# Kernel tuning notes

Hardware: AMD Instinct MI355X
Metric: run time of the kernel (lower is better)

Reference implementation:

```python
import jax, jax.numpy as jnp
import numpy as np

N_NODES = 100000
N_EDGES = 600000
D_IN = 128
D_HID = 128
BLOCKS = 3


def setup_inputs() -> dict:
    key = jax.random.key(0)
    ks = jax.random.split(key, 8)
    x = jax.random.normal(ks[0], (N_NODES, D_IN), dtype=jnp.float32)
    edge_index = jax.random.randint(ks[1], (2, N_EDGES), 0, N_NODES, dtype=jnp.int64)
    s = 1.0 / np.sqrt(D_HID)
    # MLP params per GIN block: Linear1 [hid,in], Linear2 [hid,hid] (torch layout: [out,in])
    W1 = jax.random.uniform(ks[2], (BLOCKS, D_HID, D_IN), jnp.float32, -s, s)
    b1 = jax.random.uniform(ks[3], (BLOCKS, D_HID), jnp.float32, -s, s)
    W2 = jax.random.uniform(ks[4], (BLOCKS, D_HID, D_HID), jnp.float32, -s, s)
    b2 = jax.random.uniform(ks[5], (BLOCKS, D_HID), jnp.float32, -s, s)
    Wf = jax.random.uniform(ks[6], (1, D_HID), jnp.float32, -s, s)
    bf = jax.random.uniform(ks[7], (1,), jnp.float32, -s, s)
    return {"x": x, "edge_index": edge_index, "W1": W1, "b1": b1,
            "W2": W2, "b2": b2, "Wf": Wf, "bf": bf}


def reference(x, edge_index, W1, b1, W2, b2, Wf, bf):
    src, dst = edge_index[0], edge_index[1]
    n = x.shape[0]
    h = x
    for i in range(BLOCKS):
        # GIN aggregation: (1+eps)*x_i + sum over neighbors, eps=0
        agg = jax.ops.segment_sum(h[src], dst, num_segments=n)  # [N, d]
        z = h + agg
        # 2-layer MLP inside GINConv
        z = jax.nn.relu(z @ W1[i].T + b1[i])
        z = z @ W2[i].T + b2[i]
        # outer ReLU applied in Net.forward
        h = jax.nn.relu(z)
    return h @ Wf.T + bf  # [N, 1]
```

## Files before the change

kernel.cpp:

```cpp
#include <hip/hip_runtime.h>
#include <hip/hip_bf16.h>

typedef __bf16 bf16x8 __attribute__((ext_vector_type(8)));
typedef __bf16 bf16x2 __attribute__((ext_vector_type(2)));
typedef float f32x4 __attribute__((ext_vector_type(4)));

#define NN 100000
#define DD 128
#define NE 600000
#define SLOTS 64

__global__ void convert_bf16(const float4* __restrict__ in, __bf16* __restrict__ out, int n4) {
    int i = blockIdx.x * blockDim.x + threadIdx.x;
    if (i >= n4) return;
    float4 v = in[i];
    bf16x2 a, b;
    a[0] = (__bf16)v.x; a[1] = (__bf16)v.y;
    b[0] = (__bf16)v.z; b[1] = (__bf16)v.w;
    *reinterpret_cast<bf16x2*>(out + (size_t)i * 4)     = a;
    *reinterpret_cast<bf16x2*>(out + (size_t)i * 4 + 2) = b;
}

__global__ void clear_ints(int* __restrict__ p, int n) {
    int i = blockIdx.x * blockDim.x + threadIdx.x;
    if (i < n) p[i] = 0;
}

__global__ void fill_slots(const int* __restrict__ src, const int* __restrict__ dst,
                           int* __restrict__ deg, int* __restrict__ slots, int nE) {
    int e = blockIdx.x * blockDim.x + threadIdx.x;
    if (e >= nE) return;
    int d = dst[e];
    int pos = atomicAdd(&deg[d], 1);
    if (pos < SLOTS) slots[(size_t)d * SLOTS + pos] = src[e];
}

__global__ __launch_bounds__(256) void aggregate(const __bf16* __restrict__ h,
                                                 const int* __restrict__ deg,
                                                 const int* __restrict__ slots,
                                                 __bf16* __restrict__ z, int N) {
    const int tid = threadIdx.x;
    const int grp = tid >> 4;
    const int lm  = tid & 15;
    const int n = blockIdx.x * 16 + grp;
    if (n >= N) return;
    const int off = lm * 8;

    const bf16x8 sv = *reinterpret_cast<const bf16x8*>(h + (size_t)n * DD + off);
    float acc[8];
#pragma unroll
    for (int i = 0; i < 8; ++i) acc[i] = (float)sv[i];

    int d = deg[n]; if (d > 32) d = 32;
    const int* sl = slots + (size_t)n * SLOTS;
    const int d1 = d < 16 ? d : 16;
    int myidx = (lm < d1) ? sl[lm] : 0;

    int j = 0;
    if (j + 8 <= d1) {
        int s[8];
#pragma unroll
        for (int q = 0; q < 8; ++q) s[q] = __shfl(myidx, j + q, 16);
        bf16x8 v[8];
#pragma unroll
        for (int q = 0; q < 8; ++q) v[q] = *reinterpret_cast<const bf16x8*>(h + (size_t)s[q] * DD + off);
#pragma unroll
        for (int q = 0; q < 8; ++q)
#pragma unroll
            for (int i = 0; i < 8; ++i) acc[i] += (float)v[q][i];
        j += 8;
    }
    if (j + 4 <= d1) {
        int s[4];
#pragma unroll
        for (int q = 0; q < 4; ++q) s[q] = __shfl(myidx, j + q, 16);
        bf16x8 v[4];
#pragma unroll
        for (int q = 0; q < 4; ++q) v[q] = *reinterpret_cast<const bf16x8*>(h + (size_t)s[q] * DD + off);
#pragma unroll
        for (int q = 0; q < 4; ++q)
#pragma unroll
            for (int i = 0; i < 8; ++i) acc[i] += (float)v[q][i];
        j += 4;
    }
    for (; j < d1; ++j) {
        int s = __shfl(myidx, j, 16);
        bf16x8 v = *reinterpret_cast<const bf16x8*>(h + (size_t)s * DD + off);
#pragma unroll
        for (int i = 0; i < 8; ++i) acc[i] += (float)v[i];
    }

    if (d > 16) {
        const int d2 = d - 16;
        int myidx2 = (lm < d2) ? sl[16 + lm] : 0;
        j = 0;
        if (j + 8 <= d2) {
            int s[8];
#pragma unroll
            for (int q = 0; q < 8; ++q) s[q] = __shfl(myidx2, j + q, 16);
            bf16x8 v[8];
#pragma unroll
            for (int q = 0; q < 8; ++q) v[q] = *reinterpret_cast<const bf16x8*>(h + (size_t)s[q] * DD + off);
#pragma unroll
            for (int q = 0; q < 8; ++q)
#pragma unroll
                for (int i = 0; i < 8; ++i) acc[i] += (float)v[q][i];
            j += 8;
        }
        if (j + 4 <= d2) {
            int s[4];
#pragma unroll
            for (int q = 0; q < 4; ++q) s[q] = __shfl(myidx2, j + q, 16);
            bf16x8 v[4];
#pragma unroll
            for (int q = 0; q < 4; ++q) v[q] = *reinterpret_cast<const bf16x8*>(h + (size_t)s[q] * DD + off);
#pragma unroll
            for (int q = 0; q < 4; ++q)
#pragma unroll
                for (int i = 0; i < 8; ++i) acc[i] += (float)v[q][i];
            j += 4;
        }
        for (; j < d2; ++j) {
            int s = __shfl(myidx2, j, 16);
            bf16x8 v = *reinterpret_cast<const bf16x8*>(h + (size_t)s * DD + off);
#pragma unroll
            for (int i = 0; i < 8; ++i) acc[i] += (float)v[i];
        }
    }

    bf16x8 o;
#pragma unroll
    for (int i = 0; i < 8; ++i) o[i] = (__bf16)acc[i];
    *reinterpret_cast<bf16x8*>(z + (size_t)n * DD + off) = o;
}

template<bool LAST>
__global__ __launch_bounds__(512) void mlp_fused(const __bf16* __restrict__ A,
                                                 const float* __restrict__ W1,
                                                 const float* __restrict__ b1,
                                                 const float* __restrict__ W2,
                                                 const float* __restrict__ b2,
                                                 const float* __restrict__ Wf,
                                                 const float* __restrict__ bfp,
                                                 __bf16* __restrict__ Hout,
                                                 float* __restrict__ out, int N) {
    __shared__ __bf16 w1l[128 * 136];
    __shared__ __bf16 w2l[128 * 136];
    __shared__ __bf16 tl[128 * 136];
    const int tid = threadIdx.x;

    for (int i = tid; i < 128 * 128; i += 512) {
        int r = i >> 7, c = i & 127;
        w1l[r * 136 + c] = (__bf16)W1[i];
        w2l[r * 136 + c] = (__bf16)W2[i];
    }
    __syncthreads();

    const int wave = tid >> 6;
    const int lane = tid & 63;
    const int lm = lane & 15;
    const int kg = lane >> 4;
    const int rowL = wave * 16;
    const int row0 = blockIdx.x * 128 + rowL;

    f32x4 acc[8];
#pragma unroll
    for (int c = 0; c < 8; ++c) acc[c] = (f32x4){0.f, 0.f, 0.f, 0.f};

#pragma unroll
    for (int kk = 0; kk < 4; ++kk) {
        const int kbase = kk * 32 + kg * 8;
        int r = row0 + lm;
        if (r >= N) r = N - 1;
        const bf16x8 a = *reinterpret_cast<const bf16x8*>(A + (size_t)r * DD + kbase);
#pragma unroll
        for (int c = 0; c < 8; ++c) {
            const bf16x8 b = *reinterpret_cast<const bf16x8*>(&w1l[(c * 16 + lm) * 136 + kbase]);
            acc[c] = __builtin_amdgcn_mfma_f32_16x16x32_bf16(a, b, acc[c], 0, 0, 0);
        }
    }
#pragma unroll
    for (int c = 0; c < 8; ++c) {
        const int col = c * 16 + lm;
        const float bv = b1[col];
#pragma unroll
        for (int j = 0; j < 4; ++j) {
            float v = acc[c][j] + bv;
            tl[(rowL + kg * 4 + j) * 136 + col] = (__bf16)(v > 0.f ? v : 0.f);
        }
    }
    __syncthreads();

    f32x4 acc2[8];
#pragma unroll
    for (int c = 0; c < 8; ++c) acc2[c] = (f32x4){0.f, 0.f, 0.f, 0.f};

#pragma unroll
    for (int kk = 0; kk < 4; ++kk) {
        const int kbase = kk * 32 + kg * 8;
        const bf16x8 a2 = *reinterpret_cast<const bf16x8*>(&tl[(rowL + lm) * 136 + kbase]);
#pragma unroll
        for (int c = 0; c < 8; ++c) {
            const bf16x8 b = *reinterpret_cast<const bf16x8*>(&w2l[(c * 16 + lm) * 136 + kbase]);
            acc2[c] = __builtin_amdgcn_mfma_f32_16x16x32_bf16(a2, b, acc2[c], 0, 0, 0);
        }
    }

    if (!LAST) {
        __syncthreads();
#pragma unroll
        for (int c = 0; c < 8; ++c) {
            const int col = c * 16 + lm;
            const float bv = b2[col];
#pragma unroll
            for (int j = 0; j < 4; ++j) {
                float v = acc2[c][j] + bv;
                tl[(rowL + kg * 4 + j) * 136 + col] = (__bf16)(v > 0.f ? v : 0.f);
            }
        }
        __syncthreads();
        for (int i = tid; i < 128 * 16; i += 512) {
            int r = i >> 4, cc = (i & 15) * 8;
            int gr = blockIdx.x * 128 + r;
            if (gr < N) {
                bf16x8 v = *reinterpret_cast<const bf16x8*>(&tl[r * 136 + cc]);
                *reinterpret_cast<bf16x8*>(Hout + (size_t)gr * DD + cc) = v;
            }
        }
    } else {
        float wv[8];
#pragma unroll
        for (int c = 0; c < 8; ++c) wv[c] = Wf[c * 16 + lm];
        const float bias0 = bfp[0];
#pragma unroll
        for (int j = 0; j < 4; ++j) {
            float p = 0.f;
#pragma unroll
            for (int c = 0; c < 8; ++c) {
                const int col = c * 16 + lm;
                float v = acc2[c][j] + b2[col];
                p += (v > 0.f ? v : 0.f) * wv[c];
            }
            p += __shfl_xor(p, 1, 64);
            p += __shfl_xor(p, 2, 64);
            p += __shfl_xor(p, 4, 64);
            p += __shfl_xor(p, 8, 64);
            int row = row0 + kg * 4 + j;
            if (lm == 0 && row < N) out[row] = p + bias0;
        }
    }
}

extern "C" void kernel_launch(void* const* d_in, const int* in_sizes, int n_in,
                              void* d_out, int out_size, void* d_ws, size_t ws_size,
                              hipStream_t stream) {
    const float* x  = (const float*)d_in[0];
    const int*   ei = (const int*)d_in[1];
    const float* W1 = (const float*)d_in[2];
    const float* b1 = (const float*)d_in[3];
    const float* W2 = (const float*)d_in[4];
    const float* b2 = (const float*)d_in[5];
    const float* Wf = (const float*)d_in[6];
    const float* bf = (const float*)d_in[7];
    float* out = (float*)d_out;

    const int* src = ei;
    const int* dst = ei + NE;

    __bf16* Zb   = (__bf16*)d_ws;
    __bf16* Hb   = Zb + (size_t)NN * DD;
    __bf16* Xb   = Hb + (size_t)NN * DD;
    int*  slots  = (int*)(Xb + (size_t)NN * DD);
    int*  deg    = slots + (size_t)NN * SLOTS;

    const int aggGrid = (NN + 15) / 16;
    const int mlpGrid = (NN + 127) / 128;
    const int n4 = NN * DD / 4;

    convert_bf16<<<(n4 + 255) / 256, 256, 0, stream>>>((const float4*)x, Xb, n4);
    clear_ints<<<(NN + 255) / 256, 256, 0, stream>>>(deg, NN);
    fill_slots<<<(NE + 255) / 256, 256, 0, stream>>>(src, dst, deg, slots, NE);

    aggregate<<<aggGrid, 256, 0, stream>>>(Xb, deg, slots, Zb, NN);
    mlp_fused<false><<<mlpGrid, 512, 0, stream>>>(Zb, W1, b1, W2, b2, Wf, bf, Hb, out, NN);
    aggregate<<<aggGrid, 256, 0, stream>>>(Hb, deg, slots, Zb, NN);
    mlp_fused<false><<<mlpGrid, 512, 0, stream>>>(Zb, W1 + 128 * 128, b1 + 128, W2 + 128 * 128, b2 + 128,
                                                  Wf, bf, Hb, out, NN);
    aggregate<<<aggGrid, 256, 0, stream>>>(Hb, deg, slots, Zb, NN);
    mlp_fused<true><<<mlpGrid, 512, 0, stream>>>(Zb, W1 + 2 * 128 * 128, b1 + 2 * 128, W2 + 2 * 128 * 128,
                                                 b2 + 2 * 128, Wf, bf, Hb, out, NN);
}
```

Measured before the change: 228.5 us.

## Fuse neighbor aggregation into GIN MLP kernel and prelaunch bf16 weight conversion

Merges the separate aggregate and MLP kernels into one gin_block kernel. Each block gathers neighbor sums for its 128 rows straight into shared memory, which removes the Z round trip through global memory and half the launches. Weights are converted to bf16 once by a separate kernel and read from global/L2 in the MFMA loops instead of being staged in LDS. This shrinks LDS use so more blocks can be resident, at the cost of uncoalesced global weight loads. The degree counters are also padded to a stride of 16 ints to spread the atomics, and the slot count is halved from 64 to 32.

Result: slower. 318.4 us (+39.3%).

```diff
diff --git a/kernel.cpp b/kernel.cpp
--- a/kernel.cpp
+++ b/kernel.cpp
@@ -8,7 +8,8 @@
 #define NN 100000
 #define DD 128
 #define NE 600000
-#define SLOTS 64
+#define SLOTS 32
+#define DEGSTRIDE 16
 
 __global__ void convert_bf16(const float4* __restrict__ in, __bf16* __restrict__ out, int n4) {
     int i = blockIdx.x * blockDim.x + threadIdx.x;
@@ -21,138 +22,137 @@
     *reinterpret_cast<bf16x2*>(out + (size_t)i * 4 + 2) = b;
 }
 
+__global__ void convert_w(const float* __restrict__ W1, const float* __restrict__ W2,
+                          __bf16* __restrict__ W1b, __bf16* __restrict__ W2b, int n) {
+    int i = blockIdx.x * blockDim.x + threadIdx.x;
+    if (i < n) { W1b[i] = (__bf16)W1[i]; W2b[i] = (__bf16)W2[i]; }
+}
+
 __global__ void clear_ints(int* __restrict__ p, int n) {
     int i = blockIdx.x * blockDim.x + threadIdx.x;
     if (i < n) p[i] = 0;
 }
 
 __global__ void fill_slots(const int* __restrict__ src, const int* __restrict__ dst,
-                           int* __restrict__ deg, int* __restrict__ slots, int nE) {
+                           int* __restrict__ degp, int* __restrict__ slots, int nE) {
     int e = blockIdx.x * blockDim.x + threadIdx.x;
     if (e >= nE) return;
     int d = dst[e];
-    int pos = atomicAdd(&deg[d], 1);
+    int pos = atomicAdd(&degp[(size_t)d * DEGSTRIDE], 1);
     if (pos < SLOTS) slots[(size_t)d * SLOTS + pos] = src[e];
 }
 
-__global__ __launch_bounds__(256) void aggregate(const __bf16* __restrict__ h,
-                                                 const int* __restrict__ deg,
-                                                 const int* __restrict__ slots,
-                                                 __bf16* __restrict__ z, int N) {
-    const int tid = threadIdx.x;
-    const int grp = tid >> 4;
-    const int lm  = tid & 15;
-    const int n = blockIdx.x * 16 + grp;
-    if (n >= N) return;
-    const int off = lm * 8;
-
-    const bf16x8 sv = *reinterpret_cast<const bf16x8*>(h + (size_t)n * DD + off);
-    float acc[8];
-#pragma unroll
-    for (int i = 0; i < 8; ++i) acc[i] = (float)sv[i];
-
-    int d = deg[n]; if (d > 32) d = 32;
-    const int* sl = slots + (size_t)n * SLOTS;
-    const int d1 = d < 16 ? d : 16;
-    int myidx = (lm < d1) ? sl[lm] : 0;
-
-    int j = 0;
-    if (j + 8 <= d1) {
-        int s[8];
-#pragma unroll
-        for (int q = 0; q < 8; ++q) s[q] = __shfl(myidx, j + q, 16);
-        bf16x8 v[8];
-#pragma unroll
-        for (int q = 0; q < 8; ++q) v[q] = *reinterpret_cast<const bf16x8*>(h + (size_t)s[q] * DD + off);
-#pragma unroll
-        for (int q = 0; q < 8; ++q)
-#pragma unroll
-            for (int i = 0; i < 8; ++i) acc[i] += (float)v[q][i];
-        j += 8;
-    }
-    if (j + 4 <= d1) {
-        int s[4];
-#pragma unroll
-        for (int q = 0; q < 4; ++q) s[q] = __shfl(myidx, j + q, 16);
-        bf16x8 v[4];
-#pragma unroll
-        for (int q = 0; q < 4; ++q) v[q] = *reinterpret_cast<const bf16x8*>(h + (size_t)s[q] * DD + off);
-#pragma unroll
-        for (int q = 0; q < 4; ++q)
-#pragma unroll
-            for (int i = 0; i < 8; ++i) acc[i] += (float)v[q][i];
-        j += 4;
-    }
-    for (; j < d1; ++j) {
-        int s = __shfl(myidx, j, 16);
-        bf16x8 v = *reinterpret_cast<const bf16x8*>(h + (size_t)s * DD + off);
-#pragma unroll
-        for (int i = 0; i < 8; ++i) acc[i] += (float)v[i];
-    }
-
-    if (d > 16) {
-        const int d2 = d - 16;
-        int myidx2 = (lm < d2) ? sl[16 + lm] : 0;
-        j = 0;
-        if (j + 8 <= d2) {
-            int s[8];
-#pragma unroll
-            for (int q = 0; q < 8; ++q) s[q] = __shfl(myidx2, j + q, 16);
-            bf16x8 v[8];
-#pragma unroll
-            for (int q = 0; q < 8; ++q) v[q] = *reinterpret_cast<const bf16x8*>(h + (size_t)s[q] * DD + off);
-#pragma unroll
-            for (int q = 0; q < 8; ++q)
-#pragma unroll
-                for (int i = 0; i < 8; ++i) acc[i] += (float)v[q][i];
-            j += 8;
-        }
-        if (j + 4 <= d2) {
-            int s[4];
-#pragma unroll
-            for (int q = 0; q < 4; ++q) s[q] = __shfl(myidx2, j + q, 16);
-            bf16x8 v[4];
-#pragma unroll
-            for (int q = 0; q < 4; ++q) v[q] = *reinterpret_cast<const bf16x8*>(h + (size_t)s[q] * DD + off);
-#pragma unroll
-            for (int q = 0; q < 4; ++q)
-#pragma unroll
-                for (int i = 0; i < 8; ++i) acc[i] += (float)v[q][i];
-            j += 4;
-        }
-        for (; j < d2; ++j) {
-            int s = __shfl(myidx2, j, 16);
-            bf16x8 v = *reinterpret_cast<const bf16x8*>(h + (size_t)s * DD + off);
-#pragma unroll
-            for (int i = 0; i < 8; ++i) acc[i] += (float)v[i];
-        }
-    }
-
-    bf16x8 o;
-#pragma unroll
-    for (int i = 0; i < 8; ++i) o[i] = (__bf16)acc[i];
-    *reinterpret_cast<bf16x8*>(z + (size_t)n * DD + off) = o;
-}
-
 template<bool LAST>
-__global__ __launch_bounds__(512) void mlp_fused(const __bf16* __restrict__ A,
-                                                 const float* __restrict__ W1,
-                                                 const float* __restrict__ b1,
-                                                 const float* __restrict__ W2,
-                                                 const float* __restrict__ b2,
-                                                 const float* __restrict__ Wf,
-                                                 const float* __restrict__ bfp,
-                                                 __bf16* __restrict__ Hout,
-                                                 float* __restrict__ out, int N) {
-    __shared__ __bf16 w1l[128 * 136];
-    __shared__ __bf16 w2l[128 * 136];
+__global__ __launch_bounds__(512, 4) void gin_block(const __bf16* __restrict__ Hin,
+                                                    const int* __restrict__ degp,
+                                                    const int* __restrict__ slots,
+                                                    const __bf16* __restrict__ W1b,
+                                                    const float* __restrict__ b1,
+                                                    const __bf16* __restrict__ W2b,
+                                                    const float* __restrict__ b2,
+                                                    const float* __restrict__ Wf,
+                                                    const float* __restrict__ bfp,
+                                                    __bf16* __restrict__ Hout,
+                                                    float* __restrict__ out, int N) {
     __shared__ __bf16 tl[128 * 136];
     const int tid = threadIdx.x;
 
-    for (int i = tid; i < 128 * 128; i += 512) {
-        int r = i >> 7, c = i & 127;
-        w1l[r * 136 + c] = (__bf16)W1[i];
-        w2l[r * 136 + c] = (__bf16)W2[i];
+    {
+        const int grp = tid >> 4;
+        const int lg  = tid & 15;
+        const int off = lg * 8;
+#pragma unroll
+        for (int it = 0; it < 4; ++it) {
+            const int ln = grp + (it << 5);
+            const int n = blockIdx.x * 128 + ln;
+            float acc[8] = {0.f,0.f,0.f,0.f,0.f,0.f,0.f,0.f};
+            if (n < N) {
+                const bf16x8 sv = *reinterpret_cast<const bf16x8*>(Hin + (size_t)n * DD + off);
+#pragma unroll
+                for (int i = 0; i < 8; ++i) acc[i] = (float)sv[i];
+
+                int d = degp[(size_t)n * DEGSTRIDE]; if (d > SLOTS) d = SLOTS;
+                const int* sl = slots + (size_t)n * SLOTS;
+                const int d1 = d < 16 ? d : 16;
+                int myidx = (lg < d1) ? sl[lg] : 0;
+
+                int j = 0;
+                if (j + 8 <= d1) {
+                    int s[8];
+#pragma unroll
+                    for (int q = 0; q < 8; ++q) s[q] = __shfl(myidx, j + q, 16);
+                    bf16x8 v[8];
+#pragma unroll
+                    for (int q = 0; q < 8; ++q) v[q] = *reinterpret_cast<const bf16x8*>(Hin + (size_t)s[q] * DD + off);
+#pragma unroll
+                    for (int q = 0; q < 8; ++q)
+#pragma unroll
+                        for (int i = 0; i < 8; ++i) acc[i] += (float)v[q][i];
+                    j += 8;
+                }
+                if (j + 4 <= d1) {
+                    int s[4];
+#pragma unroll
+                    for (int q = 0; q < 4; ++q) s[q] = __shfl(myidx, j + q, 16);
+                    bf16x8 v[4];
+#pragma unroll
+                    for (int q = 0; q < 4; ++q) v[q] = *reinterpret_cast<const bf16x8*>(Hin + (size_t)s[q] * DD + off);
+#pragma unroll
+                    for (int q = 0; q < 4; ++q)
+#pragma unroll
+                        for (int i = 0; i < 8; ++i) acc[i] += (float)v[q][i];
+                    j += 4;
+                }
+                for (; j < d1; ++j) {
+                    int s = __shfl(myidx, j, 16);
+                    bf16x8 v = *reinterpret_cast<const bf16x8*>(Hin + (size_t)s * DD + off);
+#pragma unroll
+                    for (int i = 0; i < 8; ++i) acc[i] += (float)v[i];
+                }
+
+                if (d > 16) {
+                    const int d2 = d - 16;
+                    int myidx2 = (lg < d2) ? sl[16 + lg] : 0;
+                    j = 0;
+                    if (j + 8 <= d2) {
+                        int s[8];
+#pragma unroll
+                        for (int q = 0; q < 8; ++q) s[q] = __shfl(myidx2, j + q, 16);
+                        bf16x8 v[8];
+#pragma unroll
+                        for (int q = 0; q < 8; ++q) v[q] = *reinterpret_cast<const bf16x8*>(Hin + (size_t)s[q] * DD + off);
+#pragma unroll
+                        for (int q = 0; q < 8; ++q)
+#pragma unroll
+                            for (int i = 0; i < 8; ++i) acc[i] += (float)v[q][i];
+                        j += 8;
+                    }
+                    if (j + 4 <= d2) {
+                        int s[4];
+#pragma unroll
+                        for (int q = 0; q < 4; ++q) s[q] = __shfl(myidx2, j + q, 16);
+                        bf16x8 v[4];
+#pragma unroll
+                        for (int q = 0; q < 4; ++q) v[q] = *reinterpret_cast<const bf16x8*>(Hin + (size_t)s[q] * DD + off);
+#pragma unroll
+                        for (int q = 0; q < 4; ++q)
+#pragma unroll
+                            for (int i = 0; i < 8; ++i) acc[i] += (float)v[q][i];
+                        j += 4;
+                    }
+                    for (; j < d2; ++j) {
+                        int s = __shfl(myidx2, j, 16);
+                        bf16x8 v = *reinterpret_cast<const bf16x8*>(Hin + (size_t)s * DD + off);
+#pragma unroll
+                        for (int i = 0; i < 8; ++i) acc[i] += (float)v[i];
+                    }
+                }
+            }
+            bf16x8 o;
+#pragma unroll
+            for (int i = 0; i < 8; ++i) o[i] = (__bf16)acc[i];
+            *reinterpret_cast<bf16x8*>(&tl[ln * 136 + off]) = o;
+        }
     }
     __syncthreads();
 
@@ -170,15 +170,14 @@
 #pragma unroll
     for (int kk = 0; kk < 4; ++kk) {
         const int kbase = kk * 32 + kg * 8;
-        int r = row0 + lm;
-        if (r >= N) r = N - 1;
-        const bf16x8 a = *reinterpret_cast<const bf16x8*>(A + (size_t)r * DD + kbase);
+        const bf16x8 a = *reinterpret_cast<const bf16x8*>(&tl[(rowL + lm) * 136 + kbase]);
 #pragma unroll
         for (int c = 0; c < 8; ++c) {
-            const bf16x8 b = *reinterpret_cast<const bf16x8*>(&w1l[(c * 16 + lm) * 136 + kbase]);
+            const bf16x8 b = *reinterpret_cast<const bf16x8*>(W1b + (size_t)(c * 16 + lm) * DD + kbase);
             acc[c] = __builtin_amdgcn_mfma_f32_16x16x32_bf16(a, b, acc[c], 0, 0, 0);
         }
     }
+    __syncthreads();
 #pragma unroll
     for (int c = 0; c < 8; ++c) {
         const int col = c * 16 + lm;
@@ -201,7 +200,7 @@
         const bf16x8 a2 = *reinterpret_cast<const bf16x8*>(&tl[(rowL + lm) * 136 + kbase]);
 #pragma unroll
         for (int c = 0; c < 8; ++c) {
-            const bf16x8 b = *reinterpret_cast<const bf16x8*>(&w2l[(c * 16 + lm) * 136 + kbase]);
+            const bf16x8 b = *reinterpret_cast<const bf16x8*>(W2b + (size_t)(c * 16 + lm) * DD + kbase);
             acc2[c] = __builtin_amdgcn_mfma_f32_16x16x32_bf16(a2, b, acc2[c], 0, 0, 0);
         }
     }
@@ -267,26 +266,29 @@
     const int* src = ei;
     const int* dst = ei + NE;
 
-    __bf16* Zb   = (__bf16*)d_ws;
-    __bf16* Hb   = Zb + (size_t)NN * DD;
-    __bf16* Xb   = Hb + (size_t)NN * DD;
-    int*  slots  = (int*)(Xb + (size_t)NN * DD);
-    int*  deg    = slots + (size_t)NN * SLOTS;
-
-    const int aggGrid = (NN + 15) / 16;
-    const int mlpGrid = (NN + 127) / 128;
+    __bf16* Xb  = (__bf16*)d_ws;
+    __bf16* Ha  = Xb + (size_t)NN * DD;
+    __bf16* Hc  = Ha + (size_t)NN * DD;
+    __bf16* W1b = Hc + (size_t)NN * DD;
+    __bf16* W2b = W1b + 3 * DD * DD;
+    int* slots  = (int*)(W2b + 3 * DD * DD);
+    int* degp   = slots + (size_t)NN * SLOTS;
+
+    const int ginGrid = (NN + 127) / 128;
     const int n4 = NN * DD / 4;
+    const int nw = 3 * DD * DD;
 
     convert_bf16<<<(n4 + 255) / 256, 256, 0, stream>>>((const float4*)x, Xb, n4);
-    clear_ints<<<(NN + 255) / 256, 256, 0, stream>>>(deg, NN);
-    fill_slots<<<(NE + 255) / 256, 256, 0, stream>>>(src, dst, deg, slots, NE);
-
-    aggregate<<<aggGrid, 256, 0, stream>>>(Xb, deg, slots, Zb, NN);
-    mlp_fused<false><<<mlpGrid, 512, 0, stream>>>(Zb, W1, b1, W2, b2, Wf, bf, Hb, out, NN);
-    aggregate<<<aggGrid, 256, 0, stream>>>(Hb, deg, slots, Zb, NN);
-    mlp_fused<false><<<mlpGrid, 512, 0, stream>>>(Zb, W1 + 128 * 128, b1 + 128, W2 + 128 * 128, b2 + 128,
-                                                  Wf, bf, Hb, out, NN);
-    aggregate<<<aggGrid, 256, 0, stream>>>(Hb, deg, slots, Zb, NN);
-    mlp_fused<true><<<mlpGrid, 512, 0, stream>>>(Zb, W1 + 2 * 128 * 128, b1 + 2 * 128, W2 + 2 * 128 * 128,
-                                                 b2 + 2 * 128, Wf, bf, Hb, out, NN);
-}
+    convert_w<<<(nw + 255) / 256, 256, 0, stream>>>(W1, W2, W1b, W2b, nw);
+    clear_ints<<<(NN * DEGSTRIDE + 255) / 256, 256, 0, stream>>>(degp, NN * DEGSTRIDE);
+    fill_slots<<<(NE + 255) / 256, 256, 0, stream>>>(src, dst, degp, slots, NE);
+
+    gin_block<false><<<ginGrid, 512, 0, stream>>>(Xb, degp, slots,
+                                                  W1b, b1, W2b, b2, Wf, bf, Ha, out, NN);
+    gin_block<false><<<ginGrid, 512, 0, stream>>>(Ha, degp, slots,
+                                                  W1b + DD * DD, b1 + DD, W2b + DD * DD, b2 + DD,
+                                                  Wf, bf, Hc, out, NN);
+    gin_block<true><<<ginGrid, 512, 0, stream>>>(Hc, degp, slots,
+                                                 W1b + 2 * DD * DD, b1 + 2 * DD, W2b + 2 * DD * DD, b2 + 2 * DD,
+                                                 Wf, bf, Ha, out, NN);
+}
```
